# Kernel optimization log

Measured on AMD Instinct MI355X. Metric: run time of the kernel, lower is better.

The kernel has to match this reference:

```python
import jax, jax.numpy as jnp
import numpy as np

B, L, C, OUT = 8, 256, 512, 512


def setup_inputs() -> dict:
    key = jax.random.key(0)
    ks = jax.random.split(key, 8)
    xd = jax.random.normal(ks[0], (B, L, C), jnp.float32)
    xt = jax.random.normal(ks[1], (B, L, C), jnp.float32)
    # Linear weights stored (in, out): y = x @ W + b (equiv. to torch x @ W^T)
    Wc = jax.random.normal(ks[2], (C, C), jnp.float32) * 0.02
    bc = jnp.zeros((C,), jnp.float32)
    Wp = jax.random.normal(ks[3], (C, C), jnp.float32) * 0.02
    bp = jnp.zeros((C,), jnp.float32)
    Wf = jax.random.normal(ks[4], (C, OUT), jnp.float32) * 0.02
    bf = jnp.zeros((OUT,), jnp.float32)
    return {"xd": xd, "xt": xt, "Wc": Wc, "bc": bc, "Wp": Wp, "bp": bp, "Wf": Wf, "bf": bf}


def reference(xd, xt, Wc, bc, Wp, bp, Wf, bf):
    # projected features
    pt = jax.nn.relu(xt) @ Wp + bp              # (b, Lt, C)
    pc = jax.nn.relu(xd) @ Wc + bc              # (b, Ld, C)
    # sigmoid bilinear scores: (b, Lt, Ld) == (b, Ld, Lt) since Lt == Ld structurally
    scores = jax.nn.sigmoid(jnp.einsum('bic,bkc->bik', pt, pc))
    # normalize by total per-batch sum
    w = scores / jnp.sum(scores, axis=(1, 2), keepdims=True)
    # tanh of elementwise outer product, reduced with attention weights
    # cp[b,c] = sum_{i,j} tanh(xd[b,i,c] * xt[b,j,c]) * w[b,i,j]
    cp = jnp.einsum('bijc,bij->bc', jnp.tanh(xd[:, :, None, :] * xt[:, None, :, :]), w)
    return cp @ Wf + bf
```

## Files before the change

### kernel.cpp

```cpp
#include <hip/hip_runtime.h>
#include <math.h>

#define B_   8
#define L_   256
#define C_   512
#define OUT_ 512

typedef _Float16 half8 __attribute__((ext_vector_type(8)));
typedef _Float16 half4 __attribute__((ext_vector_type(4)));
typedef float    f32x4 __attribute__((ext_vector_type(4)));
typedef float    f32x2 __attribute__((ext_vector_type(2)));

__global__ __launch_bounds__(256)
void proj_mfma_kernel(const float* __restrict__ xt, const float* __restrict__ Wp,
                      const float* __restrict__ bp,
                      const float* __restrict__ xd, const float* __restrict__ Wc,
                      const float* __restrict__ bc,
                      _Float16* __restrict__ pt, _Float16* __restrict__ pc)
{
    const int which = blockIdx.z;
    const float* __restrict__ X    = which ? xd : xt;
    const float* __restrict__ W    = which ? Wc : Wp;
    const float* __restrict__ bias = which ? bc : bp;
    _Float16*    __restrict__ Y    = which ? pc : pt;

    __shared__ _Float16 Ah[2][64][40];
    __shared__ _Float16 Bh[2][64][40];
    __shared__ _Float16 Ot[64][72];

    const int tid = threadIdx.x;
    const int m0 = blockIdx.y << 6, n0 = blockIdx.x << 6;
    const int lane = tid & 63, wv = tid >> 6;
    const int l15 = lane & 15, quad = lane >> 4;

    const int srow = tid >> 2, sch = (tid & 3) << 3;
    const float* Ag = X + (size_t)(m0 + srow) * C_ + sch;
    const int nl = tid & 63, kseg = tid >> 6;
    const float* Bg = W + (size_t)(kseg << 3) * C_ + n0 + nl;

    float4 a0 = *(const float4*)(Ag);
    float4 a1 = *(const float4*)(Ag + 4);
    float wr[8];
    #pragma unroll
    for (int r = 0; r < 8; ++r) wr[r] = Bg[(size_t)r * C_];

    {
        half8 av;
        av[0] = (_Float16)fmaxf(a0.x, 0.f); av[1] = (_Float16)fmaxf(a0.y, 0.f);
        av[2] = (_Float16)fmaxf(a0.z, 0.f); av[3] = (_Float16)fmaxf(a0.w, 0.f);
        av[4] = (_Float16)fmaxf(a1.x, 0.f); av[5] = (_Float16)fmaxf(a1.y, 0.f);
        av[6] = (_Float16)fmaxf(a1.z, 0.f); av[7] = (_Float16)fmaxf(a1.w, 0.f);
        *(half8*)&Ah[0][srow][sch] = av;
        half8 bv;
        #pragma unroll
        for (int r = 0; r < 8; ++r) bv[r] = (_Float16)wr[r];
        *(half8*)&Bh[0][nl][kseg << 3] = bv;
    }

    f32x4 acc[4] = {};
    for (int ks = 0; ks < 16; ++ks) {
        const int cur = ks & 1;
        if (ks < 15) {
            Ag += 32;
            Bg += 32 * C_;
            a0 = *(const float4*)(Ag);
            a1 = *(const float4*)(Ag + 4);
            #pragma unroll
            for (int r = 0; r < 8; ++r) wr[r] = Bg[(size_t)r * C_];
        }
        __syncthreads();
        half8 af = *(const half8*)&Ah[cur][(wv << 4) + l15][quad << 3];
        #pragma unroll
        for (int nb = 0; nb < 4; ++nb) {
            half8 bf = *(const half8*)&Bh[cur][(nb << 4) + l15][quad << 3];
            acc[nb] = __builtin_amdgcn_mfma_f32_16x16x32_f16(af, bf, acc[nb], 0, 0, 0);
        }
        if (ks < 15) {
            half8 av;
            av[0] = (_Float16)fmaxf(a0.x, 0.f); av[1] = (_Float16)fmaxf(a0.y, 0.f);
            av[2] = (_Float16)fmaxf(a0.z, 0.f); av[3] = (_Float16)fmaxf(a0.w, 0.f);
            av[4] = (_Float16)fmaxf(a1.x, 0.f); av[5] = (_Float16)fmaxf(a1.y, 0.f);
            av[6] = (_Float16)fmaxf(a1.z, 0.f); av[7] = (_Float16)fmaxf(a1.w, 0.f);
            *(half8*)&Ah[cur ^ 1][srow][sch] = av;
            half8 bv;
            #pragma unroll
            for (int r = 0; r < 8; ++r) bv[r] = (_Float16)wr[r];
            *(half8*)&Bh[cur ^ 1][nl][kseg << 3] = bv;
        }
    }

    __syncthreads();
    #pragma unroll
    for (int nb = 0; nb < 4; ++nb) {
        const float bz = bias[n0 + (nb << 4) + l15];
        #pragma unroll
        for (int r = 0; r < 4; ++r)
            Ot[(wv << 4) + (quad << 2) + r][(nb << 4) + l15] = (_Float16)(acc[nb][r] + bz);
    }
    __syncthreads();
    const int erow = tid >> 3, ech = (tid & 7) << 3;
    #pragma unroll
    for (int h = 0; h < 64; h += 32)
        *(half8*)&Y[(size_t)(m0 + erow + h) * C_ + n0 + ech] = *(const half8*)&Ot[erow + h][ech];
}

__device__ __forceinline__ float sigmoid_fast(float z) {
    float e = __builtin_amdgcn_exp2f(-1.4426950408889634f * z);
    return __builtin_amdgcn_rcpf(e + 1.0f);
}

__global__ __launch_bounds__(512, 4)
void cp_scores_kernel(const _Float16* __restrict__ pt, const _Float16* __restrict__ pc,
                      const float* __restrict__ xd, const float* __restrict__ xt,
                      float* __restrict__ partials, float* __restrict__ sums_part)
{
    const int bx = blockIdx.x, by = blockIdx.y, b = blockIdx.z;
    const int i0 = bx << 5, j0 = by << 5;
    const int tid = threadIdx.x;
    const int lane = tid & 63, wv = tid >> 6;
    const int l15 = lane & 15, quad = lane >> 4;

    __shared__ _Float16 Ah[2][32][40];
    __shared__ _Float16 Bh[2][32][40];
    __shared__ float ws_[32][36];
    __shared__ float wred[4];

    const int sHalf = tid >> 8;
    const int srow  = (tid & 255) >> 3;
    const int sch   = (tid & 7) << 2;
    const _Float16* Sg = (sHalf ? pc + (size_t)(b * L_ + j0 + srow) * C_
                                : pt + (size_t)(b * L_ + i0 + srow) * C_) + sch;

    half4 v = *(const half4*)Sg;
    if (sHalf) *(half4*)&Bh[0][srow][sch] = v; else *(half4*)&Ah[0][srow][sch] = v;

    f32x4 acc = {};
    for (int ks = 0; ks < 16; ++ks) {
        const int cur = ks & 1;
        if (ks < 15) { Sg += 32; v = *(const half4*)Sg; }
        __syncthreads();
        if (wv < 4) {
            half8 af = *(const half8*)&Ah[cur][((wv >> 1) << 4) + l15][quad << 3];
            half8 bf = *(const half8*)&Bh[cur][((wv & 1) << 4) + l15][quad << 3];
            acc = __builtin_amdgcn_mfma_f32_16x16x32_f16(af, bf, acc, 0, 0, 0);
        }
        if (ks < 15) {
            if (sHalf) *(half4*)&Bh[cur ^ 1][srow][sch] = v;
            else       *(half4*)&Ah[cur ^ 1][srow][sch] = v;
        }
    }

    float lsum = 0.f;
    if (wv < 4) {
        const int n = ((wv & 1) << 4) + l15;
        const int m = ((wv >> 1) << 4) + (quad << 2);
        float4 sg;
        sg.x = sigmoid_fast(acc[0]);
        sg.y = sigmoid_fast(acc[1]);
        sg.z = sigmoid_fast(acc[2]);
        sg.w = sigmoid_fast(acc[3]);
        *(float4*)&ws_[n][m] = sg;
        lsum = (sg.x + sg.y) + (sg.z + sg.w);
    }
    #pragma unroll
    for (int off = 32; off; off >>= 1) lsum += __shfl_xor(lsum, off);
    if (wv < 4 && lane == 0) wred[wv] = lsum;
    __syncthreads();
    if (tid == 0)
        sums_part[(b << 6) | (bx << 3) | by] = (wred[0] + wred[1]) + (wred[2] + wred[3]);

    const int c = tid;
    const float* __restrict__ xdb = xd + (size_t)(b * L_ + i0) * C_ + c;
    const float* __restrict__ xtb = xt + (size_t)(b * L_ + j0) * C_ + c;
    f32x2 xds2[16];
    float xtv[32];
    #pragma unroll
    for (int i = 0; i < 16; ++i) {
        xds2[i].x = xdb[(size_t)(2 * i) * C_]     * 2.8853900817779268f;
        xds2[i].y = xdb[(size_t)(2 * i + 1) * C_] * 2.8853900817779268f;
    }
    #pragma unroll
    for (int j = 0; j < 32; ++j)
        xtv[j] = xtb[(size_t)j * C_];

    f32x2 acc01 = {0.f, 0.f}, acc23 = {0.f, 0.f};
    for (int jj = 0; jj < 32; ++jj) {
        const float xv = xtv[jj];
        #pragma unroll
        for (int i = 0; i < 32; i += 4) {
            const float4 w4 = *(const float4*)&ws_[jj][i];
            f32x2 x01 = xds2[i >> 1] * xv;
            f32x2 e01 = { __builtin_amdgcn_exp2f(x01.x), __builtin_amdgcn_exp2f(x01.y) };
            f32x2 q01 = e01 + 1.0f;
            float rp01 = __builtin_amdgcn_rcpf(q01.x * q01.y);
            f32x2 r01 = rp01 * __builtin_shufflevector(q01, q01, 1, 0);
            f32x2 w01 = { w4.x, w4.y };
            acc01 = w01 * r01 + acc01;
            f32x2 x23 = xds2[(i >> 1) + 1] * xv;
            f32x2 e23 = { __builtin_amdgcn_exp2f(x23.x), __builtin_amdgcn_exp2f(x23.y) };
            f32x2 q23 = e23 + 1.0f;
            float rp23 = __builtin_amdgcn_rcpf(q23.x * q23.y);
            f32x2 r23 = rp23 * __builtin_shufflevector(q23, q23, 1, 0);
            f32x2 w23 = { w4.z, w4.w };
            acc23 = w23 * r23 + acc23;
        }
    }
    const int p = (bx << 3) | by;
    partials[(size_t)((b << 6) | p) * C_ + c] =
        (acc01.x + acc01.y) + (acc23.x + acc23.y);
}

__global__ __launch_bounds__(512)
void finalize_kernel(const float* __restrict__ partials, const float* __restrict__ sums_part,
                     const float* __restrict__ Wf, const float* __restrict__ bfv,
                     float* __restrict__ out)
{
    const int b = blockIdx.y;
    const int t = threadIdx.x;
    __shared__ float cp[C_];
    __shared__ float red[512];
    __shared__ float sumsh;

    red[t] = (t < 64) ? sums_part[(b << 6) | t] : 0.f;

    float s = 0.f;
    #pragma unroll
    for (int p = 0; p < 64; ++p)
        s += partials[(size_t)((b << 6) | p) * C_ + t];

    __syncthreads();
    for (int st = 256; st > 0; st >>= 1) {
        if (t < st) red[t] += red[t + st];
        __syncthreads();
    }
    if (t == 0) sumsh = red[0];
    __syncthreads();

    cp[t] = 1.0f - 2.0f * s / sumsh;
    __syncthreads();

    const int o  = ((int)blockIdx.x << 6) | (t & 63);
    const int c0 = (t >> 6) << 6;
    float acc = 0.f;
    #pragma unroll 8
    for (int i = 0; i < 64; ++i) {
        const int cc = c0 + i;
        acc = fmaf(cp[cc], Wf[(size_t)cc * OUT_ + o], acc);
    }
    red[t] = acc;
    __syncthreads();
    if (t < 64) {
        float a = 0.f;
        #pragma unroll
        for (int g = 0; g < 8; ++g) a += red[(g << 6) | t];
        out[(size_t)b * OUT_ + o] = a + bfv[o];
    }
}

extern "C" void kernel_launch(void* const* d_in, const int* in_sizes, int n_in,
                              void* d_out, int out_size, void* d_ws, size_t ws_size,
                              hipStream_t stream)
{
    const float* xd = (const float*)d_in[0];
    const float* xt = (const float*)d_in[1];
    const float* Wc = (const float*)d_in[2];
    const float* bc = (const float*)d_in[3];
    const float* Wp = (const float*)d_in[4];
    const float* bp = (const float*)d_in[5];
    const float* Wf = (const float*)d_in[6];
    const float* bf = (const float*)d_in[7];
    float* out = (float*)d_out;

    _Float16* pt  = (_Float16*)d_ws;
    _Float16* pc  = pt + 1048576;
    float* partials  = (float*)(pc + 1048576);
    float* sums_part = partials + B_ * 64 * C_;

    proj_mfma_kernel<<<dim3(8, 32, 2), 256, 0, stream>>>(xt, Wp, bp, xd, Wc, bc, pt, pc);
    cp_scores_kernel<<<dim3(8, 8, 8), 512, 0, stream>>>(pt, pc, xd, xt, partials, sums_part);
    finalize_kernel<<<dim3(8, 8), 512, 0, stream>>>(partials, sums_part, Wf, bf, out);
}
```

Measured before the change: 139.3 us.

## Shrink tiles in projection and cp kernels to raise block count and occupancy

```diff
diff --git a/kernel.cpp b/kernel.cpp
--- a/kernel.cpp
+++ b/kernel.cpp
@@ -24,64 +24,71 @@
     const float* __restrict__ bias = which ? bc : bp;
     _Float16*    __restrict__ Y    = which ? pc : pt;
 
-    __shared__ _Float16 Ah[2][64][40];
+    __shared__ _Float16 Ah[2][32][40];
     __shared__ _Float16 Bh[2][64][40];
-    __shared__ _Float16 Ot[64][72];
+    __shared__ _Float16 Ot[32][72];
 
     const int tid = threadIdx.x;
-    const int m0 = blockIdx.y << 6, n0 = blockIdx.x << 6;
+    const int m0 = blockIdx.y << 5, n0 = blockIdx.x << 6;
     const int lane = tid & 63, wv = tid >> 6;
     const int l15 = lane & 15, quad = lane >> 4;
+    const int mblk = wv & 1, npair = wv >> 1;
 
     const int srow = tid >> 2, sch = (tid & 3) << 3;
-    const float* Ag = X + (size_t)(m0 + srow) * C_ + sch;
+    const float* Ag = X + (size_t)(m0 + (srow & 31)) * C_ + sch;
     const int nl = tid & 63, kseg = tid >> 6;
     const float* Bg = W + (size_t)(kseg << 3) * C_ + n0 + nl;
 
-    float4 a0 = *(const float4*)(Ag);
-    float4 a1 = *(const float4*)(Ag + 4);
+    float4 a0 = {}, a1 = {};
+    if (tid < 128) { a0 = *(const float4*)(Ag); a1 = *(const float4*)(Ag + 4); }
     float wr[8];
     #pragma unroll
     for (int r = 0; r < 8; ++r) wr[r] = Bg[(size_t)r * C_];
 
-    {
+    if (tid < 128) {
         half8 av;
         av[0] = (_Float16)fmaxf(a0.x, 0.f); av[1] = (_Float16)fmaxf(a0.y, 0.f);
         av[2] = (_Float16)fmaxf(a0.z, 0.f); av[3] = (_Float16)fmaxf(a0.w, 0.f);
         av[4] = (_Float16)fmaxf(a1.x, 0.f); av[5] = (_Float16)fmaxf(a1.y, 0.f);
         av[6] = (_Float16)fmaxf(a1.z, 0.f); av[7] = (_Float16)fmaxf(a1.w, 0.f);
         *(half8*)&Ah[0][srow][sch] = av;
+    }
+    {
         half8 bv;
         #pragma unroll
         for (int r = 0; r < 8; ++r) bv[r] = (_Float16)wr[r];
         *(half8*)&Bh[0][nl][kseg << 3] = bv;
     }
 
-    f32x4 acc[4] = {};
+    f32x4 acc[2] = {};
     for (int ks = 0; ks < 16; ++ks) {
         const int cur = ks & 1;
         if (ks < 15) {
-            Ag += 32;
             Bg += 32 * C_;
-            a0 = *(const float4*)(Ag);
-            a1 = *(const float4*)(Ag + 4);
+            if (tid < 128) {
+                Ag += 32;
+                a0 = *(const float4*)(Ag);
+                a1 = *(const float4*)(Ag + 4);
+            }
             #pragma unroll
             for (int r = 0; r < 8; ++r) wr[r] = Bg[(size_t)r * C_];
         }
         __syncthreads();
-        half8 af = *(const half8*)&Ah[cur][(wv << 4) + l15][quad << 3];
-        #pragma unroll
-        for (int nb = 0; nb < 4; ++nb) {
-            half8 bf = *(const half8*)&Bh[cur][(nb << 4) + l15][quad << 3];
+        half8 af = *(const half8*)&Ah[cur][(mblk << 4) + l15][quad << 3];
+        #pragma unroll
+        for (int nb = 0; nb < 2; ++nb) {
+            half8 bf = *(const half8*)&Bh[cur][(npair << 5) + (nb << 4) + l15][quad << 3];
             acc[nb] = __builtin_amdgcn_mfma_f32_16x16x32_f16(af, bf, acc[nb], 0, 0, 0);
         }
         if (ks < 15) {
-            half8 av;
-            av[0] = (_Float16)fmaxf(a0.x, 0.f); av[1] = (_Float16)fmaxf(a0.y, 0.f);
-            av[2] = (_Float16)fmaxf(a0.z, 0.f); av[3] = (_Float16)fmaxf(a0.w, 0.f);
-            av[4] = (_Float16)fmaxf(a1.x, 0.f); av[5] = (_Float16)fmaxf(a1.y, 0.f);
-            av[6] = (_Float16)fmaxf(a1.z, 0.f); av[7] = (_Float16)fmaxf(a1.w, 0.f);
-            *(half8*)&Ah[cur ^ 1][srow][sch] = av;
+            if (tid < 128) {
+                half8 av;
+                av[0] = (_Float16)fmaxf(a0.x, 0.f); av[1] = (_Float16)fmaxf(a0.y, 0.f);
+                av[2] = (_Float16)fmaxf(a0.z, 0.f); av[3] = (_Float16)fmaxf(a0.w, 0.f);
+                av[4] = (_Float16)fmaxf(a1.x, 0.f); av[5] = (_Float16)fmaxf(a1.y, 0.f);
+                av[6] = (_Float16)fmaxf(a1.z, 0.f); av[7] = (_Float16)fmaxf(a1.w, 0.f);
+                *(half8*)&Ah[cur ^ 1][srow][sch] = av;
+            }
             half8 bv;
             #pragma unroll
             for (int r = 0; r < 8; ++r) bv[r] = (_Float16)wr[r];
@@ -91,17 +98,16 @@
 
     __syncthreads();
     #pragma unroll
-    for (int nb = 0; nb < 4; ++nb) {
-        const float bz = bias[n0 + (nb << 4) + l15];
+    for (int nb = 0; nb < 2; ++nb) {
+        const int n = (npair << 5) + (nb << 4) + l15;
+        const float bz = bias[n0 + n];
         #pragma unroll
         for (int r = 0; r < 4; ++r)
-            Ot[(wv << 4) + (quad << 2) + r][(nb << 4) + l15] = (_Float16)(acc[nb][r] + bz);
+            Ot[(mblk << 4) + (quad << 2) + r][n] = (_Float16)(acc[nb][r] + bz);
     }
     __syncthreads();
     const int erow = tid >> 3, ech = (tid & 7) << 3;
-    #pragma unroll
-    for (int h = 0; h < 64; h += 32)
-        *(half8*)&Y[(size_t)(m0 + erow + h) * C_ + n0 + ech] = *(const half8*)&Ot[erow + h][ech];
+    *(half8*)&Y[(size_t)(m0 + erow) * C_ + n0 + ech] = *(const half8*)&Ot[erow][ech];
 }
 
 __device__ __forceinline__ float sigmoid_fast(float z) {
@@ -109,83 +115,82 @@
     return __builtin_amdgcn_rcpf(e + 1.0f);
 }
 
-__global__ __launch_bounds__(512, 4)
+__global__ __launch_bounds__(256, 6)
 void cp_scores_kernel(const _Float16* __restrict__ pt, const _Float16* __restrict__ pc,
                       const float* __restrict__ xd, const float* __restrict__ xt,
                       float* __restrict__ partials, float* __restrict__ sums_part)
 {
-    const int bx = blockIdx.x, by = blockIdx.y, b = blockIdx.z;
-    const int i0 = bx << 5, j0 = by << 5;
+    const int bx = blockIdx.x, by = blockIdx.y;
+    const int b = blockIdx.z >> 1, ch = blockIdx.z & 1;
+    const int i0 = bx << 5, j0 = by << 4;
     const int tid = threadIdx.x;
     const int lane = tid & 63, wv = tid >> 6;
     const int l15 = lane & 15, quad = lane >> 4;
 
     __shared__ _Float16 Ah[2][32][40];
-    __shared__ _Float16 Bh[2][32][40];
-    __shared__ float ws_[32][36];
-    __shared__ float wred[4];
-
-    const int sHalf = tid >> 8;
-    const int srow  = (tid & 255) >> 3;
-    const int sch   = (tid & 7) << 2;
-    const _Float16* Sg = (sHalf ? pc + (size_t)(b * L_ + j0 + srow) * C_
-                                : pt + (size_t)(b * L_ + i0 + srow) * C_) + sch;
-
-    half4 v = *(const half4*)Sg;
-    if (sHalf) *(half4*)&Bh[0][srow][sch] = v; else *(half4*)&Ah[0][srow][sch] = v;
+    __shared__ _Float16 Bh[2][16][40];
+    __shared__ float ws_[16][36];
+    __shared__ float wred[2];
+
+    const int srow = tid >> 2;
+    const int sch  = (tid & 3) << 3;
+    const _Float16* Sg = ((srow < 32) ? pt + (size_t)(b * L_ + i0 + srow) * C_
+                                      : pc + (size_t)(b * L_ + j0 + (srow - 32)) * C_) + sch;
+
+    half8 v = {};
+    if (tid < 192) v = *(const half8*)Sg;
+    if (tid < 192) {
+        if (srow < 32) *(half8*)&Ah[0][srow][sch] = v;
+        else           *(half8*)&Bh[0][srow - 32][sch] = v;
+    }
 
     f32x4 acc = {};
     for (int ks = 0; ks < 16; ++ks) {
         const int cur = ks & 1;
-        if (ks < 15) { Sg += 32; v = *(const half4*)Sg; }
+        if (ks < 15 && tid < 192) { Sg += 32; v = *(const half8*)Sg; }
         __syncthreads();
-        if (wv < 4) {
-            half8 af = *(const half8*)&Ah[cur][((wv >> 1) << 4) + l15][quad << 3];
-            half8 bf = *(const half8*)&Bh[cur][((wv & 1) << 4) + l15][quad << 3];
+        if (wv < 2) {
+            half8 af = *(const half8*)&Ah[cur][(wv << 4) + l15][quad << 3];
+            half8 bf = *(const half8*)&Bh[cur][l15][quad << 3];
             acc = __builtin_amdgcn_mfma_f32_16x16x32_f16(af, bf, acc, 0, 0, 0);
         }
-        if (ks < 15) {
-            if (sHalf) *(half4*)&Bh[cur ^ 1][srow][sch] = v;
-            else       *(half4*)&Ah[cur ^ 1][srow][sch] = v;
+        if (ks < 15 && tid < 192) {
+            if (srow < 32) *(half8*)&Ah[cur ^ 1][srow][sch] = v;
+            else           *(half8*)&Bh[cur ^ 1][srow - 32][sch] = v;
         }
     }
 
     float lsum = 0.f;
-    if (wv < 4) {
-        const int n = ((wv & 1) << 4) + l15;
-        const int m = ((wv >> 1) << 4) + (quad << 2);
+    if (wv < 2) {
         float4 sg;
         sg.x = sigmoid_fast(acc[0]);
         sg.y = sigmoid_fast(acc[1]);
         sg.z = sigmoid_fast(acc[2]);
         sg.w = sigmoid_fast(acc[3]);
-        *(float4*)&ws_[n][m] = sg;
+        *(float4*)&ws_[l15][(wv << 4) + (quad << 2)] = sg;
         lsum = (sg.x + sg.y) + (sg.z + sg.w);
     }
     #pragma unroll
     for (int off = 32; off; off >>= 1) lsum += __shfl_xor(lsum, off);
-    if (wv < 4 && lane == 0) wred[wv] = lsum;
-    __syncthreads();
-    if (tid == 0)
-        sums_part[(b << 6) | (bx << 3) | by] = (wred[0] + wred[1]) + (wred[2] + wred[3]);
-
-    const int c = tid;
+    if (wv < 2 && lane == 0) wred[wv] = lsum;
+    __syncthreads();
+    if (tid == 0 && ch == 0)
+        sums_part[(b << 7) | (bx << 4) | by] = wred[0] + wred[1];
+
+    const int c = (ch << 8) | tid;
     const float* __restrict__ xdb = xd + (size_t)(b * L_ + i0) * C_ + c;
     const float* __restrict__ xtb = xt + (size_t)(b * L_ + j0) * C_ + c;
     f32x2 xds2[16];
-    float xtv[32];
     #pragma unroll
     for (int i = 0; i < 16; ++i) {
         xds2[i].x = xdb[(size_t)(2 * i) * C_]     * 2.8853900817779268f;
         xds2[i].y = xdb[(size_t)(2 * i + 1) * C_] * 2.8853900817779268f;
     }
-    #pragma unroll
-    for (int j = 0; j < 32; ++j)
-        xtv[j] = xtb[(size_t)j * C_];
 
     f32x2 acc01 = {0.f, 0.f}, acc23 = {0.f, 0.f};
-    for (int jj = 0; jj < 32; ++jj) {
-        const float xv = xtv[jj];
+    #pragma unroll 4
+    for (int jj = 0; jj < 16; ++jj) {
+        const float xv = xtb[(size_t)jj * C_];
         #pragma unroll
         for (int i = 0; i < 32; i += 4) {
             const float4 w4 = *(const float4*)&ws_[jj][i];
@@ -205,8 +210,8 @@
             acc23 = w23 * r23 + acc23;
         }
     }
-    const int p = (bx << 3) | by;
-    partials[(size_t)((b << 6) | p) * C_ + c] =
+    const int p = (bx << 4) | by;
+    partials[(size_t)((b << 7) | p) * C_ + c] =
         (acc01.x + acc01.y) + (acc23.x + acc23.y);
 }
 
@@ -221,12 +226,12 @@
     __shared__ float red[512];
     __shared__ float sumsh;
 
-    red[t] = (t < 64) ? sums_part[(b << 6) | t] : 0.f;
+    red[t] = (t < 128) ? sums_part[(b << 7) | t] : 0.f;
 
     float s = 0.f;
     #pragma unroll
-    for (int p = 0; p < 64; ++p)
-        s += partials[(size_t)((b << 6) | p) * C_ + t];
+    for (int p = 0; p < 128; ++p)
+        s += partials[(size_t)((b << 7) | p) * C_ + t];
 
     __syncthreads();
     for (int st = 256; st > 0; st >>= 1) {
@@ -274,9 +279,9 @@
     _Float16* pt  = (_Float16*)d_ws;
     _Float16* pc  = pt + 1048576;
     float* partials  = (float*)(pc + 1048576);
-    float* sums_part = partials + B_ * 64 * C_;
-
-    proj_mfma_kernel<<<dim3(8, 32, 2), 256, 0, stream>>>(xt, Wp, bp, xd, Wc, bc, pt, pc);
-    cp_scores_kernel<<<dim3(8, 8, 8), 512, 0, stream>>>(pt, pc, xd, xt, partials, sums_part);
+    float* sums_part = partials + B_ * 128 * C_;
+
+    proj_mfma_kernel<<<dim3(8, 64, 2), 256, 0, stream>>>(xt, Wp, bp, xd, Wc, bc, pt, pc);
+    cp_scores_kernel<<<dim3(8, 16, 16), 256, 0, stream>>>(pt, pc, xd, xt, partials, sums_part);
     finalize_kernel<<<dim3(8, 8), 512, 0, stream>>>(partials, sums_part, Wf, bf, out);
 }
```

Result: slower. 143.8 us (+3.2%).
